# Kernel tuning notes

Measured on AMD Instinct MI355X. Metric: run time of the kernel, lower is better.

## Reference

```python
import jax, jax.numpy as jnp
import numpy as np

B, C, H, W = 32, 512, 40, 40
NC = 20
STRIDE = 32
CONF_THRESH = 0.3
NMS_THRESH = 0.5


def setup_inputs() -> dict:
    key = jax.random.key(0)
    ks = jax.random.split(key, 7)
    # 0.02 scale on weights keeps sigmoid/exp in a realistic, non-saturated range
    return {
        "feat": jax.random.normal(ks[0], (B, C, H, W), dtype=jnp.float32),
        "w_obj": jax.random.normal(ks[1], (1, C), dtype=jnp.float32) * 0.02,
        "b_obj": jnp.zeros((1,), dtype=jnp.float32),
        "w_cls": jax.random.normal(ks[2], (NC, C), dtype=jnp.float32) * 0.02,
        "b_cls": jnp.zeros((NC,), dtype=jnp.float32),
        "w_reg": jax.random.normal(ks[3], (4, C), dtype=jnp.float32) * 0.02,
        "b_reg": jnp.zeros((4,), dtype=jnp.float32),
    }


def _pairwise_iou(b):  # b: [N,4] xyxy
    area = (b[:, 2] - b[:, 0]) * (b[:, 3] - b[:, 1])
    x1 = jnp.maximum(b[:, None, 0], b[None, :, 0])
    y1 = jnp.maximum(b[:, None, 1], b[None, :, 1])
    x2 = jnp.minimum(b[:, None, 2], b[None, :, 2])
    y2 = jnp.minimum(b[:, None, 3], b[None, :, 3])
    inter = jnp.maximum(x2 - x1, 0.0) * jnp.maximum(y2 - y1, 0.0)
    union = area[:, None] + area[None, :] - inter
    return inter / union


def _nms_single(boxes, scores, labels, conf_mask):
    # Greedy per-class NMS with fixed shapes (keep mask), matching the
    # original: suppression happens only among boxes of the same class
    # that pass conf_thresh, in descending score order.
    N = boxes.shape[0]
    order = jnp.argsort(-scores)
    b = boxes[order]
    l = labels[order]
    v = conf_mask[order]
    iou = _pairwise_iou(b)  # [N,N]
    idx = jnp.arange(N)
    later = idx[None, :] > idx[:, None]
    sup = (iou > NMS_THRESH) & (l[:, None] == l[None, :]) & later

    def body(i, keep):
        # if box i is still kept, suppress all later same-class overlaps
        return keep & ~(sup[i] & keep[i])

    keep_sorted = jax.lax.fori_loop(0, N, body, v)
    return jnp.zeros((N,), dtype=bool).at[order].set(keep_sorted)


def reference(feat, w_obj, b_obj, w_cls, b_cls, w_reg, b_reg):
    Bn, Cc, Hh, Ww = feat.shape
    N = Hh * Ww
    # permute(0,2,3,1).flatten(1,2) -> [B, H*W, C]
    x = feat.transpose(0, 2, 3, 1).reshape(Bn, N, Cc)
    # 1x1 convs == per-cell linear layers
    obj = jnp.einsum("bnc,oc->bno", x, w_obj) + b_obj  # [B,N,1]
    cls = jnp.einsum("bnc,oc->bno", x, w_cls) + b_cls  # [B,N,NC]
    reg = jnp.einsum("bnc,oc->bno", x, w_reg) + b_reg  # [B,N,4]
    # decode_boxes
    gy, gx = jnp.meshgrid(jnp.arange(Hh), jnp.arange(Ww), indexing="ij")
    grid = jnp.stack([gx, gy], axis=-1).reshape(-1, 2).astype(feat.dtype)  # [N,2]
    ctr = (jax.nn.sigmoid(reg[..., :2]) + grid) * STRIDE
    wh = jnp.exp(reg[..., 2:]) * STRIDE
    boxes = jnp.concatenate([ctr - wh * 0.5, ctr + wh * 0.5], axis=-1)  # [B,N,4]
    # scores = sqrt(sigmoid(obj) * sigmoid(cls)); per-cell best class
    sc = jnp.sqrt(jax.nn.sigmoid(obj) * jax.nn.sigmoid(cls))  # [B,N,NC]
    scores = sc.max(axis=-1)
    labels = jnp.argmax(sc, axis=-1)
    conf_mask = scores > CONF_THRESH
    keep = jax.vmap(_nms_single)(boxes, scores, labels, conf_mask)  # [B,N]
    out = jnp.concatenate(
        [jnp.where(keep[..., None], boxes, 0.0),
         jnp.where(keep, scores, 0.0)[..., None]],
        axis=-1,
    )  # [B,N,5]
    return out, labels, keep
```

## Files before the change

### kernel.cpp

```cpp
#include <hip/hip_runtime.h>
#include <stdint.h>
#include <stddef.h>

#define Bn 32
#define Cc 512
#define Hh 40
#define Ww 40
#define Npix 1600
#define NCx 20
#define NCELL (Bn*Npix)
#define CONF 0.3f
#define NMS_T 0.5f
#define NOUT 25

#define CB 64
#define BPI 25
#define NWAVE 4
#define CR (Cc/NWAVE)

#define WS_WT     0
#define WS_BOXES  (WS_WT + (size_t)NOUT*Cc)
#define WS_SCORES (WS_BOXES + (size_t)NCELL*4)
#define WS_LABELS (WS_SCORES + (size_t)NCELL)

__device__ __forceinline__ float sigmoidf_(float x) {
    return 1.0f / (1.0f + expf(-x));
}

__global__ __launch_bounds__(64) void k0_pack(
    const float* __restrict__ w_obj, const float* __restrict__ w_cls,
    const float* __restrict__ w_reg, float* __restrict__ Wt)
{
    int c = blockIdx.x * 64 + threadIdx.x;
    if (c < Cc) {
        Wt[c] = w_obj[c];
        #pragma unroll
        for (int o = 0; o < NCx; ++o) Wt[(size_t)(1 + o) * Cc + c] = w_cls[o * Cc + c];
        #pragma unroll
        for (int o = 0; o < 4; ++o)   Wt[(size_t)(21 + o) * Cc + c] = w_reg[o * Cc + c];
    }
}

__global__ __launch_bounds__(256) void k1_fused(
    const float* __restrict__ feat, const float* __restrict__ Wt,
    const float* __restrict__ b_obj, const float* __restrict__ b_cls,
    const float* __restrict__ b_reg,
    float* __restrict__ out, float* __restrict__ ws_boxes,
    float* __restrict__ ws_scores, int* __restrict__ ws_labels)
{
    __shared__ float red[NWAVE][NOUT][CB];

    const int tid = threadIdx.x;
    const int w   = __builtin_amdgcn_readfirstlane(tid >> 6);
    const int l   = tid & 63;
    const int b   = blockIdx.x / BPI;
    const int j   = blockIdx.x % BPI;
    const int n0  = j * CB;

    {
        const float* fp = feat + (size_t)b * (Cc * Npix) + (size_t)(w * CR) * Npix + (n0 + l);
        float x[CR];
        #pragma unroll
        for (int cc = 0; cc < CR; ++cc) x[cc] = fp[(size_t)cc * Npix];

        const float* wt0 = Wt + w * CR;
        #pragma unroll
        for (int q = 0; q < 5; ++q) {
            const float* w0 = wt0 + (size_t)(5 * q + 0) * Cc;
            const float* w1 = wt0 + (size_t)(5 * q + 1) * Cc;
            const float* w2 = wt0 + (size_t)(5 * q + 2) * Cc;
            const float* w3 = wt0 + (size_t)(5 * q + 3) * Cc;
            const float* w4 = wt0 + (size_t)(5 * q + 4) * Cc;
            float a0 = 0.f, a1 = 0.f, a2 = 0.f, a3 = 0.f, a4 = 0.f;
            #pragma unroll
            for (int cc = 0; cc < CR; ++cc) {
                float xv = x[cc];
                a0 = fmaf(xv, w0[cc], a0);
                a1 = fmaf(xv, w1[cc], a1);
                a2 = fmaf(xv, w2[cc], a2);
                a3 = fmaf(xv, w3[cc], a3);
                a4 = fmaf(xv, w4[cc], a4);
            }
            red[w][5 * q + 0][l] = a0;
            red[w][5 * q + 1][l] = a1;
            red[w][5 * q + 2][l] = a2;
            red[w][5 * q + 3][l] = a3;
            red[w][5 * q + 4][l] = a4;
        }
    }
    __syncthreads();

    if (tid < CB) {
        float v[NOUT];
        #pragma unroll
        for (int o = 0; o < NOUT; ++o) v[o] = red[0][o][tid];
        #pragma unroll
        for (int ch = 1; ch < NWAVE; ++ch) {
            #pragma unroll
            for (int o = 0; o < NOUT; ++o) v[o] += red[ch][o][tid];
        }

        float obj = v[0] + b_obj[0];
        float m = -1e30f; int label = 0;
        #pragma unroll
        for (int o = 0; o < NCx; ++o) {
            float cv = v[1 + o] + b_cls[o];
            if (cv > m) { m = cv; label = o; }
        }
        float r0 = v[21] + b_reg[0], r1 = v[22] + b_reg[1];
        float r2 = v[23] + b_reg[2], r3 = v[24] + b_reg[3];

        int n = n0 + tid;
        int g = b * Npix + n;
        int gy = n / Ww, gx = n % Ww;
        float cx = (sigmoidf_(r0) + (float)gx) * 32.0f;
        float cy = (sigmoidf_(r1) + (float)gy) * 32.0f;
        float bw = expf(r2) * 32.0f;
        float bh = expf(r3) * 32.0f;
        float x1 = cx - bw * 0.5f, y1 = cy - bh * 0.5f;
        float x2 = cx + bw * 0.5f, y2 = cy + bh * 0.5f;
        float score = sqrtf(sigmoidf_(obj) * sigmoidf_(m));

        ((float4*)ws_boxes)[g] = make_float4(x1, y1, x2, y2);
        ws_scores[g] = score;
        ws_labels[g] = label;

        float* orow = out + (size_t)g * 5;
        orow[0] = 0.f; orow[1] = 0.f; orow[2] = 0.f; orow[3] = 0.f; orow[4] = 0.f;
        out[(size_t)NCELL * 5 + g] = (float)label;
        out[(size_t)NCELL * 6 + g] = 0.f;
    }
}

#define KSUP 320
#define WUMAX ((KSUP + 31) / 32)

__global__ __launch_bounds__(256) void k3_nms(
    const float4* __restrict__ ws_boxes, const float* __restrict__ ws_scores,
    const int* __restrict__ ws_labels, float* __restrict__ out)
{
    __shared__ unsigned int cnt;
    __shared__ unsigned long long keys[2048];
    __shared__ float bx1[Npix], by1[Npix], bx2[Npix], by2[Npix], bar[Npix];
    __shared__ unsigned int sup[KSUP * WUMAX];
    __shared__ unsigned int keepbits[WUMAX];

    const int tid = threadIdx.x;
    const int b   = blockIdx.x / NCx;
    const int cls = blockIdx.x % NCx;
    const int gbase = b * Npix;

    if (tid == 0) cnt = 0;
    __syncthreads();

    for (int n = tid; n < Npix; n += 256) {
        float s = ws_scores[gbase + n];
        if (s > CONF && ws_labels[gbase + n] == cls) {
            unsigned int pos = atomicAdd(&cnt, 1u);
            unsigned int sb = __float_as_uint(s);
            keys[pos] = ((unsigned long long)(~sb) << 32) | (unsigned int)n;
        }
    }
    __syncthreads();
    const int k = (int)cnt;
    if (k == 0) return;

    int M = 2; while (M < k) M <<= 1;
    for (int s = tid; s < M; s += 256) if (s >= k) keys[s] = ~0ull;
    __syncthreads();

    for (int sz = 2; sz <= M; sz <<= 1) {
        for (int st = sz >> 1; st > 0; st >>= 1) {
            for (int t = tid; t < M; t += 256) {
                int p = t ^ st;
                if (p > t) {
                    unsigned long long a = keys[t], c = keys[p];
                    bool up = ((t & sz) == 0);
                    if (up ? (a > c) : (a < c)) { keys[t] = c; keys[p] = a; }
                }
            }
            __syncthreads();
        }
    }

    for (int s = tid; s < k; s += 256) {
        int n = (int)(unsigned int)keys[s];
        float4 bx = ws_boxes[gbase + n];
        bx1[s] = bx.x; by1[s] = bx.y; bx2[s] = bx.z; by2[s] = bx.w;
        bar[s] = (bx.z - bx.x) * (bx.w - bx.y);
    }
    __syncthreads();

    if (k <= KSUP) {
        const int wu = (k + 31) >> 5;
        for (int t = tid; t < k * wu; t += 256) {
            int i = t / wu, w = t - (t / wu) * wu;
            unsigned int bits = 0;
            int j0 = w << 5;
            float xi1 = bx1[i], yi1 = by1[i], xi2 = bx2[i], yi2 = by2[i], ai = bar[i];
            for (int jj = 0; jj < 32; ++jj) {
                int j = j0 + jj;
                if (j > i && j < k) {
                    float xx1 = fmaxf(xi1, bx1[j]);
                    float yy1 = fmaxf(yi1, by1[j]);
                    float xx2 = fminf(xi2, bx2[j]);
                    float yy2 = fminf(yi2, by2[j]);
                    float inter = fmaxf(xx2 - xx1, 0.f) * fmaxf(yy2 - yy1, 0.f);
                    float uni = ai + bar[j] - inter;
                    if (inter / uni > NMS_T) bits |= (1u << jj);
                }
            }
            sup[i * wu + w] = bits;
        }
        if (tid < wu) {
            int rem = k - (tid << 5);
            keepbits[tid] = (rem >= 32) ? 0xFFFFFFFFu : ((1u << rem) - 1u);
        }
        __syncthreads();

        if (tid < 64) {
            for (int i = 0; i < k; ++i) {
                unsigned int cur = keepbits[i >> 5];
                if ((cur >> (i & 31)) & 1u) {
                    if (tid < wu) keepbits[tid] &= ~sup[i * wu + tid];
                }
            }
            unsigned int* keepF = sup;
            for (int s2 = tid; s2 < k; s2 += 64)
                keepF[s2] = (keepbits[s2 >> 5] >> (s2 & 31)) & 1u;
        }
        __syncthreads();
    } else {
        unsigned int* keepF = sup;
        for (int s = tid; s < k; s += 256) keepF[s] = 1u;
        __syncthreads();
        for (int i = 0; i < k; ++i) {
            __syncthreads();
            if (keepF[i]) {
                float xi1 = bx1[i], yi1 = by1[i], xi2 = bx2[i], yi2 = by2[i], ai = bar[i];
                for (int j = i + 1 + tid; j < k; j += 256) {
                    float xx1 = fmaxf(xi1, bx1[j]);
                    float yy1 = fmaxf(yi1, by1[j]);
                    float xx2 = fminf(xi2, bx2[j]);
                    float yy2 = fminf(yi2, by2[j]);
                    float inter = fmaxf(xx2 - xx1, 0.f) * fmaxf(yy2 - yy1, 0.f);
                    float uni = ai + bar[j] - inter;
                    if (inter / uni > NMS_T) keepF[j] = 0u;
                }
            }
        }
        __syncthreads();
    }

    unsigned int* keepF = sup;
    for (int s = tid; s < k; s += 256) {
        if (keepF[s]) {
            int n = (int)(unsigned int)keys[s];
            unsigned int sb = ~(unsigned int)(keys[s] >> 32);
            float sc = __uint_as_float(sb);
            float* orow = out + (size_t)(gbase + n) * 5;
            orow[0] = bx1[s]; orow[1] = by1[s];
            orow[2] = bx2[s]; orow[3] = by2[s];
            orow[4] = sc;
            out[(size_t)NCELL * 6 + gbase + n] = 1.0f;
        }
    }
}

extern "C" void kernel_launch(void* const* d_in, const int* in_sizes, int n_in,
                              void* d_out, int out_size, void* d_ws, size_t ws_size,
                              hipStream_t stream) {
    const float* feat  = (const float*)d_in[0];
    const float* w_obj = (const float*)d_in[1];
    const float* b_obj = (const float*)d_in[2];
    const float* w_cls = (const float*)d_in[3];
    const float* b_cls = (const float*)d_in[4];
    const float* w_reg = (const float*)d_in[5];
    const float* b_reg = (const float*)d_in[6];
    float* out = (float*)d_out;
    float* ws  = (float*)d_ws;

    float* Wt     = ws + WS_WT;
    float* boxes  = ws + WS_BOXES;
    float* scores = ws + WS_SCORES;
    int*   labels = (int*)(ws + WS_LABELS);

    k0_pack<<<(Cc + 63) / 64, 64, 0, stream>>>(w_obj, w_cls, w_reg, Wt);
    k1_fused<<<Bn * BPI, 256, 0, stream>>>(feat, Wt, b_obj, b_cls, b_reg,
                                           out, boxes, scores, labels);
    k3_nms<<<Bn * NCx, 256, 0, stream>>>((const float4*)boxes, scores, labels, out);
}
```

Measured before the change: 240.5 us.

## Stream feature channels in double-buffered batches instead of loading all into registers

Each wave used to load all 128 channel values per pixel into registers before doing the 25 dot products. Now it keeps 25 accumulators and streams the channels in batches of 8 with two ping-pong buffers, so the next batch's loads overlap the current batch's FMAs. This is meant to cut register pressure, which may have been causing spills or low occupancy, and to hide global load latency. The loop is no longer fully unrolled, which adds some loop overhead and changes the order in which weights are read.

```diff
diff --git a/kernel.cpp b/kernel.cpp
--- a/kernel.cpp
+++ b/kernel.cpp
@@ -17,6 +17,7 @@
 #define BPI 25
 #define NWAVE 4
 #define CR (Cc/NWAVE)
+#define FB 8
 
 #define WS_WT     0
 #define WS_BOXES  (WS_WT + (size_t)NOUT*Cc)
@@ -38,6 +39,23 @@
         for (int o = 0; o < NCx; ++o) Wt[(size_t)(1 + o) * Cc + c] = w_cls[o * Cc + c];
         #pragma unroll
         for (int o = 0; o < 4; ++o)   Wt[(size_t)(21 + o) * Cc + c] = w_reg[o * Cc + c];
+    }
+}
+
+__device__ __forceinline__ void ld_batch(float dst[FB], const float* __restrict__ fp,
+                                         int base) {
+    #pragma unroll
+    for (int t = 0; t < FB; ++t) dst[t] = fp[(size_t)(base + t) * Npix];
+}
+
+__device__ __forceinline__ void fma_batch(float acc[NOUT], const float x[FB],
+                                          const float* __restrict__ wt0, int base) {
+    #pragma unroll
+    for (int o = 0; o < NOUT; ++o) {
+        const float* wr = wt0 + (size_t)o * Cc + base;
+        #pragma unroll
+        for (int t = 0; t < FB; ++t)
+            acc[o] = fmaf(x[t], wr[t], acc[o]);
     }
 }
 
@@ -58,35 +76,28 @@
     const int n0  = j * CB;
 
     {
-        const float* fp = feat + (size_t)b * (Cc * Npix) + (size_t)(w * CR) * Npix + (n0 + l);
-        float x[CR];
-        #pragma unroll
-        for (int cc = 0; cc < CR; ++cc) x[cc] = fp[(size_t)cc * Npix];
-
+        const float* fp  = feat + (size_t)b * (Cc * Npix) + (size_t)(w * CR) * Npix + (n0 + l);
         const float* wt0 = Wt + w * CR;
-        #pragma unroll
-        for (int q = 0; q < 5; ++q) {
-            const float* w0 = wt0 + (size_t)(5 * q + 0) * Cc;
-            const float* w1 = wt0 + (size_t)(5 * q + 1) * Cc;
-            const float* w2 = wt0 + (size_t)(5 * q + 2) * Cc;
-            const float* w3 = wt0 + (size_t)(5 * q + 3) * Cc;
-            const float* w4 = wt0 + (size_t)(5 * q + 4) * Cc;
-            float a0 = 0.f, a1 = 0.f, a2 = 0.f, a3 = 0.f, a4 = 0.f;
-            #pragma unroll
-            for (int cc = 0; cc < CR; ++cc) {
-                float xv = x[cc];
-                a0 = fmaf(xv, w0[cc], a0);
-                a1 = fmaf(xv, w1[cc], a1);
-                a2 = fmaf(xv, w2[cc], a2);
-                a3 = fmaf(xv, w3[cc], a3);
-                a4 = fmaf(xv, w4[cc], a4);
-            }
-            red[w][5 * q + 0][l] = a0;
-            red[w][5 * q + 1][l] = a1;
-            red[w][5 * q + 2][l] = a2;
-            red[w][5 * q + 3][l] = a3;
-            red[w][5 * q + 4][l] = a4;
-        }
+
+        float acc[NOUT];
+        #pragma unroll
+        for (int o = 0; o < NOUT; ++o) acc[o] = 0.f;
+
+        float xa[FB], xb[FB];
+        ld_batch(xa, fp, 0);
+        int base = 0;
+        for (; base < CR - 2 * FB; base += 2 * FB) {
+            ld_batch(xb, fp, base + FB);
+            fma_batch(acc, xa, wt0, base);
+            ld_batch(xa, fp, base + 2 * FB);
+            fma_batch(acc, xb, wt0, base + FB);
+        }
+        ld_batch(xb, fp, base + FB);
+        fma_batch(acc, xa, wt0, base);
+        fma_batch(acc, xb, wt0, base + FB);
+
+        #pragma unroll
+        for (int o = 0; o < NOUT; ++o) red[w][o][l] = acc[o];
     }
     __syncthreads();
 
```

New measurement: 248.4 us. +3.3%, slower.
